# Kernel tuning notes

Hardware: AMD Instinct MI355X
Metric: run time of the kernel (lower is better)

The kernel has to match this reference:

```python
import jax, jax.numpy as jnp
import numpy as np
import math

B, S, E, HEAD = 4, 2048, 1024, 64  # num_heads=16 -> head_size = 1024//16


def setup_inputs() -> dict:
    key = jax.random.key(0)
    kx, kp, kq, kk, kv = jax.random.split(key, 5)
    std = math.sqrt(2.0 / (E + HEAD))
    return {
        "x": jax.random.normal(kx, (B, S, E), dtype=jnp.float32),
        "padding_mask": jax.random.randint(kp, (B, S), 0, 2, dtype=jnp.int32),
        "Wq": jax.random.normal(kq, (HEAD, E), dtype=jnp.float32) * std,
        "Wk": jax.random.normal(kk, (HEAD, E), dtype=jnp.float32) * std,
        "Wv": jax.random.normal(kv, (HEAD, E), dtype=jnp.float32) * std,
    }


def reference(x, padding_mask, Wq, Wk, Wv):
    # q,k,v: [B,S,head] via Linear (x @ W.T, no bias)
    q = jnp.einsum("bse,he->bsh", x, Wq)
    k = jnp.einsum("bse,he->bsh", x, Wk)
    v = jnp.einsum("bse,he->bsh", x, Wv)
    scores = jnp.einsum("bqh,bkh->bqk", q, k)  # [B,S,S]
    seq = x.shape[1]
    causal = jnp.tril(jnp.ones((seq, seq), dtype=jnp.float32))  # [S,S]
    mask = causal[None, :, :] * padding_mask.astype(jnp.float32)[:, None, :]  # [B,S,S]
    scores = jnp.where(mask == 0, jnp.float32(-1e9), scores)
    head_size = k.shape[-1]
    attn = jax.nn.softmax(scores / jnp.sqrt(jnp.float32(head_size)), axis=-1)
    return jnp.einsum("bqk,bkh->bqh", attn, v)
```

## Files before the change

kernel.cpp:

```cpp
#include <hip/hip_runtime.h>
#include <hip/hip_bf16.h>
#include <math.h>

#define B_ 4
#define S_ 2048
#define E_ 1024
#define H_ 64
#define NQT 32
#define SPLITS 8
#define TPS 4

typedef short bf16x8 __attribute__((ext_vector_type(8)));
typedef float f32x4 __attribute__((ext_vector_type(4)));
typedef unsigned short u16x8 __attribute__((ext_vector_type(8)));
typedef unsigned short u16x4 __attribute__((ext_vector_type(4)));

__device__ __forceinline__ unsigned short f2bf(float f){
    unsigned u = __builtin_bit_cast(unsigned, f);
    u += 0x7fffu + ((u >> 16) & 1u);
    return (unsigned short)(u >> 16);
}
__device__ __forceinline__ float bf2f(unsigned short h){
    return __builtin_bit_cast(float, ((unsigned)h) << 16);
}
#define MFMA16(a,b,c) __builtin_amdgcn_mfma_f32_16x16x32_bf16((a),(b),(c),0,0,0)

__device__ __forceinline__ void gload_lds16(const void* g, void* l){
    __builtin_amdgcn_global_load_lds((const __attribute__((address_space(1))) unsigned int*)g,
                                     (__attribute__((address_space(3))) unsigned int*)l, 16, 0, 0);
}

__global__ __launch_bounds__(256) void wprep_kernel(
    const float* __restrict__ Wq, const float* __restrict__ Wk,
    const float* __restrict__ Wv,
    unsigned short* __restrict__ WhiS, unsigned short* __restrict__ WloS)
{
    const int gid = blockIdx.x*256 + threadIdx.x;
    const int n = gid >> 7, g = gid & 127;
    const float* W = (n < 64)  ? (Wq + (size_t)n*E_)
                   : (n < 128) ? (Wk + (size_t)(n-64)*E_)
                               : (Wv + (size_t)(n-128)*E_);
    const int gs = (g & ~7) | ((g & 7) ^ (n & 7));
    const float* src = W + gs*8;
    float4 a = ((const float4*)src)[0];
    float4 b = ((const float4*)src)[1];
    float vv[8] = {a.x,a.y,a.z,a.w,b.x,b.y,b.z,b.w};
    u16x8 hv, lv;
    #pragma unroll
    for (int j=0;j<8;j++){ unsigned short h = f2bf(vv[j]); hv[j]=h; lv[j]=f2bf(vv[j]-bf2f(h)); }
    ((u16x8*)WhiS)[n*128 + g] = hv;
    ((u16x8*)WloS)[n*128 + g] = lv;
}

__global__ __launch_bounds__(256) void qkv_kernel(
    const float* __restrict__ x,
    const unsigned short* __restrict__ WhiS, const unsigned short* __restrict__ WloS,
    unsigned short* __restrict__ Qhi, unsigned short* __restrict__ Qlo,
    unsigned short* __restrict__ Khi, unsigned short* __restrict__ Klo,
    unsigned short* __restrict__ Vt)
{
    __shared__ unsigned short Ah[32*64], Al[32*64];
    __shared__ unsigned short Bh[192*64], Bl[192*64];
    const int m0 = blockIdx.x * 32;
    const int tid = threadIdx.x;
    const int lane = tid & 63, wv = tid >> 6, l15 = lane & 15, quad = lane >> 4;

    f32x4 acc[2][3];
    #pragma unroll
    for (int mt=0;mt<2;mt++)
    #pragma unroll
    for (int nt=0;nt<3;nt++) acc[mt][nt] = f32x4{0.f,0.f,0.f,0.f};

    const int arow = tid >> 3;
    const int ag   = tid & 7;
    unsigned short* tbuf = (wv < 2) ? Bh : Bl;
    const unsigned short* gsrc = (wv < 2) ? WhiS : WloS;
    const int rbase0 = (wv & 1) * 96;
    const int lrow = lane >> 3, lgrp = lane & 7;

    for (int k0 = 0; k0 < E_; k0 += 64) {
        const float* xs = x + (size_t)(m0 + arow)*E_ + k0 + ag*8;
        float4 xa = ((const float4*)xs)[0];
        float4 xb = ((const float4*)xs)[1];
        __syncthreads();
        #pragma unroll
        for (int i = 0; i < 12; i++) {
            const int rb = rbase0 + i*8;
            const unsigned short* gp = gsrc + (size_t)(rb + lrow)*E_ + k0 + lgrp*8;
            gload_lds16(gp, tbuf + rb*64);
        }
        {
            float vv[8] = {xa.x,xa.y,xa.z,xa.w,xb.x,xb.y,xb.z,xb.w};
            u16x8 hv, lv;
            #pragma unroll
            for (int j=0;j<8;j++){ unsigned short h = f2bf(vv[j]); hv[j]=h; lv[j]=f2bf(vv[j]-bf2f(h)); }
            const int idx = arow*8 + (ag ^ (arow & 7));
            ((u16x8*)Ah)[idx] = hv; ((u16x8*)Al)[idx] = lv;
        }
        __syncthreads();
        #pragma unroll
        for (int kk=0; kk<2; kk++){
            const int xr = (kk*4+quad) ^ (l15 & 7);
            bf16x8 ah[2], al[2];
            #pragma unroll
            for (int mt=0; mt<2; mt++){
                const int arw = mt*16 + l15;
                ah[mt] = ((const bf16x8*)Ah)[arw*8 + xr];
                al[mt] = ((const bf16x8*)Al)[arw*8 + xr];
            }
            #pragma unroll
            for (int nt=0; nt<3; nt++){
                const int brw = wv*48 + nt*16 + l15;
                bf16x8 bh = ((const bf16x8*)Bh)[brw*8 + xr];
                bf16x8 bl = ((const bf16x8*)Bl)[brw*8 + xr];
                #pragma unroll
                for (int mt=0; mt<2; mt++){
                    acc[mt][nt] = MFMA16(ah[mt], bh, acc[mt][nt]);
                    acc[mt][nt] = MFMA16(ah[mt], bl, acc[mt][nt]);
                    acc[mt][nt] = MFMA16(al[mt], bh, acc[mt][nt]);
                }
            }
        }
    }
    #pragma unroll
    for (int nt=0; nt<3; nt++){
        const int n = wv*48 + nt*16 + l15;
        const int comp = n >> 6, c = n & 63;
        if (comp < 2) {
            unsigned short* dh = (comp==0) ? Qhi : Khi;
            unsigned short* dl = (comp==0) ? Qlo : Klo;
            #pragma unroll
            for (int mt=0; mt<2; mt++)
            #pragma unroll
            for (int r=0; r<4; r++){
                const int row = m0 + mt*16 + quad*4 + r;
                float v = acc[mt][nt][r];
                unsigned short h = f2bf(v);
                dh[(size_t)row*H_ + c] = h;
                dl[(size_t)row*H_ + c] = f2bf(v - bf2f(h));
            }
        } else {
            #pragma unroll
            for (int mt=0; mt<2; mt++){
                const int m = m0 + mt*16 + quad*4;
                const int b = m >> 11, s0 = m & (S_-1);
                u16x4 pk;
                #pragma unroll
                for (int r=0;r<4;r++) pk[r] = f2bf(acc[mt][nt][r]);
                *(u16x4*)(Vt + (size_t)(b*H_ + c)*S_ + s0) = pk;
            }
        }
    }
}

__global__ __launch_bounds__(256) void meanv_kernel(const unsigned short* __restrict__ Vt,
                                                    float* __restrict__ meanV)
{
    int b = blockIdx.x >> 6, h = blockIdx.x & 63;
    const unsigned short* src = Vt + (size_t)b*H_*S_ + (size_t)h*S_;
    float sum = 0.f;
    for (int j = threadIdx.x; j < S_; j += 256) sum += bf2f(src[j]);
    #pragma unroll
    for (int m=32; m>=1; m>>=1) sum += __shfl_xor(sum, m);
    __shared__ float red[4];
    if ((threadIdx.x & 63) == 0) red[threadIdx.x >> 6] = sum;
    __syncthreads();
    if (threadIdx.x == 0) meanV[b*H_ + h] = (red[0]+red[1]+red[2]+red[3]) * (1.f/S_);
}

__global__ __launch_bounds__(256) void attn_kernel(
    const unsigned short* __restrict__ Qhi, const unsigned short* __restrict__ Qlo,
    const unsigned short* __restrict__ Khi, const unsigned short* __restrict__ Klo,
    const unsigned short* __restrict__ Vt, const int* __restrict__ pad,
    float* __restrict__ Opart, float* __restrict__ mpart, float* __restrict__ lpart)
{
    const int qt = blockIdx.x, b = blockIdx.y, sp = blockIdx.z;
    const int t0 = sp * TPS;
    if (t0 > qt) return;
    const int t1 = min(t0 + TPS, qt + 1);

    __shared__ unsigned short Ps[4][64*20];

    const int tid = threadIdx.x, lane = tid & 63, wv = tid >> 6, l15 = lane & 15, quad = lane >> 4;

    const size_t qrow = (size_t)(b*S_ + qt*64 + wv*16 + l15);
    bf16x8 aqh0 = *(const bf16x8*)(Qhi + qrow*H_ + quad*8);
    bf16x8 aqh1 = *(const bf16x8*)(Qhi + qrow*H_ + 32 + quad*8);
    bf16x8 aql0 = *(const bf16x8*)(Qlo + qrow*H_ + quad*8);
    bf16x8 aql1 = *(const bf16x8*)(Qlo + qrow*H_ + 32 + quad*8);

    const unsigned short* KhB = Khi + (size_t)(b*S_)*H_;
    const unsigned short* KlB = Klo + (size_t)(b*S_)*H_;
    const unsigned short* VB  = Vt  + (size_t)b*H_*S_;
    const int* padB = pad + b*S_;

    float m_i[4], l_i[4];
    f32x4 o[4];
    #pragma unroll
    for (int r=0;r<4;r++){ m_i[r] = -INFINITY; l_i[r] = 0.f; }
    #pragma unroll
    for (int i=0;i<4;i++) o[i] = f32x4{0.f,0.f,0.f,0.f};

    const int qg = qt*64 + wv*16 + quad*4;
    unsigned short* Pw = &Ps[wv][0];

    for (int t = t0; t < t1; ++t) {
        const int kb = t * 64;

        int pv[4];
        #pragma unroll
        for (int nt=0; nt<4; nt++) pv[nt] = padB[kb + nt*16 + l15];

        f32x4 s[4];
        #pragma unroll
        for (int nt=0; nt<4; nt++){
            const size_t krow = (size_t)(kb + nt*16 + l15)*H_;
            bf16x8 bh0 = *(const bf16x8*)(KhB + krow + quad*8);
            bf16x8 bh1 = *(const bf16x8*)(KhB + krow + 32 + quad*8);
            bf16x8 bl0 = *(const bf16x8*)(KlB + krow + quad*8);
            bf16x8 bl1 = *(const bf16x8*)(KlB + krow + 32 + quad*8);
            f32x4 z = f32x4{0.f,0.f,0.f,0.f};
            z = MFMA16(aqh0, bh0, z);
            z = MFMA16(aqh1, bh1, z);
            z = MFMA16(aqh0, bl0, z);
            z = MFMA16(aqh1, bl1, z);
            z = MFMA16(aql0, bh0, z);
            z = MFMA16(aql1, bh1, z);
            s[nt] = z;
        }
        float rmax[4] = {-INFINITY,-INFINITY,-INFINITY,-INFINITY};
        #pragma unroll
        for (int nt=0; nt<4; nt++){
            const int kg = kb + nt*16 + l15;
            #pragma unroll
            for (int r=0;r<4;r++){
                bool ok = (kg <= qg + r) && (pv[nt] != 0);
                float v = ok ? s[nt][r]*0.125f : -1.25e8f;
                s[nt][r] = v;
                rmax[r] = fmaxf(rmax[r], v);
            }
        }
        #pragma unroll
        for (int msk=1; msk<=8; msk<<=1){
            #pragma unroll
            for (int r=0;r<4;r++) rmax[r] = fmaxf(rmax[r], __shfl_xor(rmax[r], msk));
        }
        float alpha[4];
        #pragma unroll
        for (int r=0;r<4;r++){
            float mn = fmaxf(m_i[r], rmax[r]);
            alpha[r] = __expf(m_i[r] - mn);
            m_i[r] = mn;
        }
        float rsum[4] = {0.f,0.f,0.f,0.f};
        #pragma unroll
        for (int nt=0; nt<4; nt++)
        #pragma unroll
        for (int r=0;r<4;r++){
            float p = __expf(s[nt][r] - m_i[r]);
            s[nt][r] = p;
            rsum[r] += p;
        }
        #pragma unroll
        for (int msk=1; msk<=8; msk<<=1){
            #pragma unroll
            for (int r=0;r<4;r++) rsum[r] += __shfl_xor(rsum[r], msk);
        }
        #pragma unroll
        for (int r=0;r<4;r++) l_i[r] = l_i[r]*alpha[r] + rsum[r];
        #pragma unroll
        for (int hnt=0; hnt<4; hnt++)
        #pragma unroll
        for (int r=0;r<4;r++) o[hnt][r] *= alpha[r];

        #pragma unroll
        for (int nt=0; nt<4; nt++){
            const int key = nt*16 + l15;
            u16x4 pk;
            #pragma unroll
            for (int r=0;r<4;r++) pk[r] = f2bf(s[nt][r]);
            *(u16x4*)(Pw + key*20 + quad*4) = pk;
        }
        #pragma unroll
        for (int ks=0; ks<2; ks++){
            bf16x8 ap;
            #pragma unroll
            for (int j=0;j<8;j++) ap[j] = (short)Pw[(ks*32 + quad*8 + j)*20 + l15];
            #pragma unroll
            for (int hnt=0; hnt<4; hnt++){
                bf16x8 bv = *(const bf16x8*)(VB + (size_t)(hnt*16 + l15)*S_ + kb + ks*32 + quad*8);
                o[hnt] = MFMA16(ap, bv, o[hnt]);
            }
        }
    }
    const size_t rbase = ((size_t)((b*NQT + qt)*SPLITS + sp))*64 + wv*16 + quad*4;
    if (l15 == 0) {
        #pragma unroll
        for (int r=0;r<4;r++){ mpart[rbase + r] = m_i[r]; lpart[rbase + r] = l_i[r]; }
    }
    #pragma unroll
    for (int hnt=0; hnt<4; hnt++)
    #pragma unroll
    for (int r=0;r<4;r++)
        Opart[(rbase + r)*H_ + hnt*16 + l15] = o[hnt][r];
}

__global__ __launch_bounds__(256) void combine_kernel(
    const float* __restrict__ Opart, const float* __restrict__ mpart,
    const float* __restrict__ lpart, const float* __restrict__ meanV,
    float* __restrict__ out)
{
    const int idx = blockIdx.x*256 + threadIdx.x;
    const int h = idx & 63;
    const int q = (idx >> 6) & (S_-1);
    const int b = idx >> 17;
    const int qt = q >> 6, r = q & 63;
    const int ns = (qt >> 2) + 1;
    const size_t rb = ((size_t)(b*NQT + qt)*SPLITS)*64 + r;
    float M = -INFINITY;
    for (int s2=0; s2<ns; s2++) M = fmaxf(M, mpart[rb + (size_t)s2*64]);
    float res;
    if (M == -1.25e8f) {
        res = meanV[b*H_ + h];
    } else {
        float L = 0.f, acc = 0.f;
        for (int s2=0; s2<ns; s2++){
            float mi = mpart[rb + (size_t)s2*64];
            float wgt = __expf(mi - M);
            L += wgt * lpart[rb + (size_t)s2*64];
            acc += wgt * Opart[(rb + (size_t)s2*64)*H_ + h];
        }
        res = acc / L;
    }
    out[idx] = res;
}

extern "C" void kernel_launch(void* const* d_in, const int* in_sizes, int n_in,
                              void* d_out, int out_size, void* d_ws, size_t ws_size,
                              hipStream_t stream)
{
    (void)in_sizes; (void)n_in; (void)out_size; (void)ws_size;
    const float* x  = (const float*)d_in[0];
    const int* pad  = (const int*)d_in[1];
    const float* Wq = (const float*)d_in[2];
    const float* Wk = (const float*)d_in[3];
    const float* Wv = (const float*)d_in[4];
    float* out = (float*)d_out;
    char* ws = (char*)d_ws;
    const size_t MB = 1u << 20;
    unsigned short* Qhi = (unsigned short*)(ws + 0*MB);
    unsigned short* Qlo = (unsigned short*)(ws + 1*MB);
    unsigned short* Khi = (unsigned short*)(ws + 2*MB);
    unsigned short* Klo = (unsigned short*)(ws + 3*MB);
    unsigned short* Vt  = (unsigned short*)(ws + 4*MB);
    float* Opart = (float*)(ws + 5*MB);
    float* mpart = (float*)(ws + 21*MB);
    float* lpart = (float*)(ws + 21*MB + (1u<<18));
    float* meanV = (float*)(ws + 21*MB + 2*(1u<<18));
    unsigned short* WhiS = (unsigned short*)(ws + 22*MB);
    unsigned short* WloS = (unsigned short*)(ws + 22*MB + 512*1024);

    wprep_kernel<<<dim3(96), 256, 0, stream>>>(Wq, Wk, Wv, WhiS, WloS);
    qkv_kernel<<<dim3(256), 256, 0, stream>>>(x, WhiS, WloS, Qhi, Qlo, Khi, Klo, Vt);
    meanv_kernel<<<dim3(256), 256, 0, stream>>>(Vt, meanV);
    attn_kernel<<<dim3(NQT, B_, SPLITS), 256, 0, stream>>>(Qhi, Qlo, Khi, Klo, Vt, pad,
                                                           Opart, mpart, lpart);
    combine_kernel<<<dim3((B_*S_*H_)/256), 256, 0, stream>>>(Opart, mpart, lpart, meanV, out);
}
```

Baseline: 162.2 us.

## Double-buffer QKV and attention tiles in LDS, swizzle layouts, drop meanV kernel

The QKV projection now double-buffers its A and B tiles in LDS, so the loads for the next K-chunk overlap the MFMAs on the current one. The attention kernel stages the K hi/lo, V and padding tiles into LDS with per-wave roles, double-buffered, instead of reading fragments straight from global memory. Q, K and V are stored in XOR-swizzled layouts to cut LDS bank conflicts. The causal compare now runs only on the diagonal tile. The separate mean-V kernel is removed, and fully masked rows compute the V mean inline in the combine kernel, which is costly per thread but only for rare rows.

```diff
diff --git a/kernel.cpp b/kernel.cpp
--- a/kernel.cpp
+++ b/kernel.cpp
@@ -29,6 +29,7 @@
     __builtin_amdgcn_global_load_lds((const __attribute__((address_space(1))) unsigned int*)g,
                                      (__attribute__((address_space(3))) unsigned int*)l, 16, 0, 0);
 }
+
 
 __global__ __launch_bounds__(256) void wprep_kernel(
     const float* __restrict__ Wq, const float* __restrict__ Wk,
@@ -59,8 +60,8 @@
     unsigned short* __restrict__ Khi, unsigned short* __restrict__ Klo,
     unsigned short* __restrict__ Vt)
 {
-    __shared__ unsigned short Ah[32*64], Al[32*64];
-    __shared__ unsigned short Bh[192*64], Bl[192*64];
+    __shared__ unsigned short Ah[2][32*64], Al[2][32*64];
+    __shared__ unsigned short Bh[2][192*64], Bl[2][192*64];
     const int m0 = blockIdx.x * 32;
     const int tid = threadIdx.x;
     const int lane = tid & 63, wv = tid >> 6, l15 = lane & 15, quad = lane >> 4;
@@ -73,31 +74,39 @@
 
     const int arow = tid >> 3;
     const int ag   = tid & 7;
-    unsigned short* tbuf = (wv < 2) ? Bh : Bl;
     const unsigned short* gsrc = (wv < 2) ? WhiS : WloS;
     const int rbase0 = (wv & 1) * 96;
     const int lrow = lane >> 3, lgrp = lane & 7;
 
-    for (int k0 = 0; k0 < E_; k0 += 64) {
+    float4 xa, xb;
+    auto loadx = [&](int k0){
         const float* xs = x + (size_t)(m0 + arow)*E_ + k0 + ag*8;
-        float4 xa = ((const float4*)xs)[0];
-        float4 xb = ((const float4*)xs)[1];
-        __syncthreads();
+        xa = ((const float4*)xs)[0];
+        xb = ((const float4*)xs)[1];
+    };
+    auto stageB = [&](int buf, int k0){
+        unsigned short* tb = (wv < 2) ? &Bh[buf][0] : &Bl[buf][0];
         #pragma unroll
         for (int i = 0; i < 12; i++) {
             const int rb = rbase0 + i*8;
-            const unsigned short* gp = gsrc + (size_t)(rb + lrow)*E_ + k0 + lgrp*8;
-            gload_lds16(gp, tbuf + rb*64);
-        }
-        {
-            float vv[8] = {xa.x,xa.y,xa.z,xa.w,xb.x,xb.y,xb.z,xb.w};
-            u16x8 hv, lv;
-            #pragma unroll
-            for (int j=0;j<8;j++){ unsigned short h = f2bf(vv[j]); hv[j]=h; lv[j]=f2bf(vv[j]-bf2f(h)); }
-            const int idx = arow*8 + (ag ^ (arow & 7));
-            ((u16x8*)Ah)[idx] = hv; ((u16x8*)Al)[idx] = lv;
-        }
-        __syncthreads();
+            gload_lds16(gsrc + (size_t)(rb + lrow)*E_ + k0 + lgrp*8, tb + rb*64);
+        }
+    };
+    auto writeA = [&](int buf){
+        float vv[8] = {xa.x,xa.y,xa.z,xa.w,xb.x,xb.y,xb.z,xb.w};
+        u16x8 hv, lv;
+        #pragma unroll
+        for (int j=0;j<8;j++){ unsigned short h = f2bf(vv[j]); hv[j]=h; lv[j]=f2bf(vv[j]-bf2f(h)); }
+        const int idx = arow*8 + (ag ^ (arow & 7));
+        ((u16x8*)&Ah[buf][0])[idx] = hv; ((u16x8*)&Al[buf][0])[idx] = lv;
+    };
+
+    loadx(0); stageB(0, 0); writeA(0);
+    __syncthreads();
+
+    for (int k = 0; k < 16; k++) {
+        const int c = k & 1;
+        if (k < 15) { loadx((k+1)*64); stageB(c^1, (k+1)*64); }
         #pragma unroll
         for (int kk=0; kk<2; kk++){
             const int xr = (kk*4+quad) ^ (l15 & 7);
@@ -105,14 +114,14 @@
             #pragma unroll
             for (int mt=0; mt<2; mt++){
                 const int arw = mt*16 + l15;
-                ah[mt] = ((const bf16x8*)Ah)[arw*8 + xr];
-                al[mt] = ((const bf16x8*)Al)[arw*8 + xr];
+                ah[mt] = ((const bf16x8*)&Ah[c][0])[arw*8 + xr];
+                al[mt] = ((const bf16x8*)&Al[c][0])[arw*8 + xr];
             }
             #pragma unroll
             for (int nt=0; nt<3; nt++){
                 const int brw = wv*48 + nt*16 + l15;
-                bf16x8 bh = ((const bf16x8*)Bh)[brw*8 + xr];
-                bf16x8 bl = ((const bf16x8*)Bl)[brw*8 + xr];
+                bf16x8 bh = ((const bf16x8*)&Bh[c][0])[brw*8 + xr];
+                bf16x8 bl = ((const bf16x8*)&Bl[c][0])[brw*8 + xr];
                 #pragma unroll
                 for (int mt=0; mt<2; mt++){
                     acc[mt][nt] = MFMA16(ah[mt], bh, acc[mt][nt]);
@@ -121,11 +130,16 @@
                 }
             }
         }
+        if (k < 15) {
+            writeA(c^1);
+            __syncthreads();
+        }
     }
+
     #pragma unroll
     for (int nt=0; nt<3; nt++){
         const int n = wv*48 + nt*16 + l15;
-        const int comp = n >> 6, c = n & 63;
+        const int comp = n >> 6, cidx = n & 63;
         if (comp < 2) {
             unsigned short* dh = (comp==0) ? Qhi : Khi;
             unsigned short* dl = (comp==0) ? Qlo : Klo;
@@ -134,38 +148,26 @@
             #pragma unroll
             for (int r=0; r<4; r++){
                 const int row = m0 + mt*16 + quad*4 + r;
+                const int csw = (((cidx >> 3) ^ (row & 7)) << 3) | (cidx & 7);
                 float v = acc[mt][nt][r];
                 unsigned short h = f2bf(v);
-                dh[(size_t)row*H_ + c] = h;
-                dl[(size_t)row*H_ + c] = f2bf(v - bf2f(h));
+                dh[(size_t)row*H_ + csw] = h;
+                dl[(size_t)row*H_ + csw] = f2bf(v - bf2f(h));
             }
         } else {
             #pragma unroll
             for (int mt=0; mt<2; mt++){
                 const int m = m0 + mt*16 + quad*4;
                 const int b = m >> 11, s0 = m & (S_-1);
+                const int g = s0 >> 3;
+                const int pg = (g & ~7) | ((g ^ (cidx & 7)) & 7);
                 u16x4 pk;
                 #pragma unroll
                 for (int r=0;r<4;r++) pk[r] = f2bf(acc[mt][nt][r]);
-                *(u16x4*)(Vt + (size_t)(b*H_ + c)*S_ + s0) = pk;
+                *(u16x4*)(Vt + ((size_t)b*H_ + cidx)*S_ + pg*8 + (s0 & 7)) = pk;
             }
         }
     }
-}
-
-__global__ __launch_bounds__(256) void meanv_kernel(const unsigned short* __restrict__ Vt,
-                                                    float* __restrict__ meanV)
-{
-    int b = blockIdx.x >> 6, h = blockIdx.x & 63;
-    const unsigned short* src = Vt + (size_t)b*H_*S_ + (size_t)h*S_;
-    float sum = 0.f;
-    for (int j = threadIdx.x; j < S_; j += 256) sum += bf2f(src[j]);
-    #pragma unroll
-    for (int m=32; m>=1; m>>=1) sum += __shfl_xor(sum, m);
-    __shared__ float red[4];
-    if ((threadIdx.x & 63) == 0) red[threadIdx.x >> 6] = sum;
-    __syncthreads();
-    if (threadIdx.x == 0) meanV[b*H_ + h] = (red[0]+red[1]+red[2]+red[3]) * (1.f/S_);
 }
 
 __global__ __launch_bounds__(256) void attn_kernel(
@@ -179,15 +181,21 @@
     if (t0 > qt) return;
     const int t1 = min(t0 + TPS, qt + 1);
 
+    __shared__ unsigned short KtH[2][64*64], KtL[2][64*64], Vts[2][64*64];
     __shared__ unsigned short Ps[4][64*20];
+    __shared__ int pad_s[2][64];
 
     const int tid = threadIdx.x, lane = tid & 63, wv = tid >> 6, l15 = lane & 15, quad = lane >> 4;
+    const int role = wv;
 
     const size_t qrow = (size_t)(b*S_ + qt*64 + wv*16 + l15);
-    bf16x8 aqh0 = *(const bf16x8*)(Qhi + qrow*H_ + quad*8);
-    bf16x8 aqh1 = *(const bf16x8*)(Qhi + qrow*H_ + 32 + quad*8);
-    bf16x8 aql0 = *(const bf16x8*)(Qlo + qrow*H_ + quad*8);
-    bf16x8 aql1 = *(const bf16x8*)(Qlo + qrow*H_ + 32 + quad*8);
+    const int xk = l15 & 7;
+    const unsigned short* qbh = Qhi + qrow*H_;
+    const unsigned short* qbl = Qlo + qrow*H_;
+    bf16x8 aqh0 = *(const bf16x8*)(qbh + ((quad     ^ xk) << 3));
+    bf16x8 aqh1 = *(const bf16x8*)(qbh + (((4+quad) ^ xk) << 3));
+    bf16x8 aql0 = *(const bf16x8*)(qbl + ((quad     ^ xk) << 3));
+    bf16x8 aql1 = *(const bf16x8*)(qbl + (((4+quad) ^ xk) << 3));
 
     const unsigned short* KhB = Khi + (size_t)(b*S_)*H_;
     const unsigned short* KlB = Klo + (size_t)(b*S_)*H_;
@@ -204,21 +212,50 @@
     const int qg = qt*64 + wv*16 + quad*4;
     unsigned short* Pw = &Ps[wv][0];
 
+    auto stage = [&](int buf, int t){
+        const int kb = t * 64;
+        if (role == 0){
+            const unsigned short* g = KhB + (size_t)kb*H_;
+            unsigned short* l = &KtH[buf][0];
+            #pragma unroll
+            for (int j=0;j<8;j++) gload_lds16(g + j*512 + lane*8, l + j*512);
+        } else if (role == 1){
+            const unsigned short* g = KlB + (size_t)kb*H_;
+            unsigned short* l = &KtL[buf][0];
+            #pragma unroll
+            for (int j=0;j<8;j++) gload_lds16(g + j*512 + lane*8, l + j*512);
+        } else if (role == 2){
+            unsigned short* l = &Vts[buf][0];
+            const unsigned short* g = VB + (size_t)(lane>>3)*S_ + kb + (lane&7)*8;
+            #pragma unroll
+            for (int j=0;j<8;j++) gload_lds16(g + (size_t)j*8*S_, l + j*512);
+        } else {
+            pad_s[buf][lane] = padB[kb + lane];
+        }
+    };
+
+    stage(0, t0);
+    __syncthreads();
+
     for (int t = t0; t < t1; ++t) {
+        const int c = (t - t0) & 1;
         const int kb = t * 64;
+        if (t + 1 < t1) stage(c^1, t+1);
 
         int pv[4];
         #pragma unroll
-        for (int nt=0; nt<4; nt++) pv[nt] = padB[kb + nt*16 + l15];
-
+        for (int nt=0; nt<4; nt++) pv[nt] = pad_s[c][nt*16 + l15];
+
+        const bf16x8* KH = (const bf16x8*)&KtH[c][0];
+        const bf16x8* KL = (const bf16x8*)&KtL[c][0];
         f32x4 s[4];
         #pragma unroll
         for (int nt=0; nt<4; nt++){
-            const size_t krow = (size_t)(kb + nt*16 + l15)*H_;
-            bf16x8 bh0 = *(const bf16x8*)(KhB + krow + quad*8);
-            bf16x8 bh1 = *(const bf16x8*)(KhB + krow + 32 + quad*8);
-            bf16x8 bl0 = *(const bf16x8*)(KlB + krow + quad*8);
-            bf16x8 bl1 = *(const bf16x8*)(KlB + krow + 32 + quad*8);
+            const int krw = nt*16 + l15;
+            bf16x8 bh0 = KH[krw*8 + ((quad)   ^ xk)];
+            bf16x8 bh1 = KH[krw*8 + ((4+quad) ^ xk)];
+            bf16x8 bl0 = KL[krw*8 + ((quad)   ^ xk)];
+            bf16x8 bl1 = KL[krw*8 + ((4+quad) ^ xk)];
             f32x4 z = f32x4{0.f,0.f,0.f,0.f};
             z = MFMA16(aqh0, bh0, z);
             z = MFMA16(aqh1, bh1, z);
@@ -229,15 +266,28 @@
             s[nt] = z;
         }
         float rmax[4] = {-INFINITY,-INFINITY,-INFINITY,-INFINITY};
-        #pragma unroll
-        for (int nt=0; nt<4; nt++){
-            const int kg = kb + nt*16 + l15;
-            #pragma unroll
-            for (int r=0;r<4;r++){
-                bool ok = (kg <= qg + r) && (pv[nt] != 0);
-                float v = ok ? s[nt][r]*0.125f : -1.25e8f;
-                s[nt][r] = v;
-                rmax[r] = fmaxf(rmax[r], v);
+        if (t == qt) {
+            #pragma unroll
+            for (int nt=0; nt<4; nt++){
+                const int kg = kb + nt*16 + l15;
+                #pragma unroll
+                for (int r=0;r<4;r++){
+                    bool ok = (kg <= qg + r) && (pv[nt] != 0);
+                    float v = ok ? s[nt][r]*0.125f : -1.25e8f;
+                    s[nt][r] = v;
+                    rmax[r] = fmaxf(rmax[r], v);
+                }
+            }
+        } else {
+            #pragma unroll
+            for (int nt=0; nt<4; nt++){
+                const bool ok = (pv[nt] != 0);
+                #pragma unroll
+                for (int r=0;r<4;r++){
+                    float v = ok ? s[nt][r]*0.125f : -1.25e8f;
+                    s[nt][r] = v;
+                    rmax[r] = fmaxf(rmax[r], v);
+                }
             }
         }
         #pragma unroll
@@ -281,6 +331,7 @@
             for (int r=0;r<4;r++) pk[r] = f2bf(s[nt][r]);
             *(u16x4*)(Pw + key*20 + quad*4) = pk;
         }
+        const bf16x8* VS = (const bf16x8*)&Vts[c][0];
         #pragma unroll
         for (int ks=0; ks<2; ks++){
             bf16x8 ap;
@@ -288,10 +339,12 @@
             for (int j=0;j<8;j++) ap[j] = (short)Pw[(ks*32 + quad*8 + j)*20 + l15];
             #pragma unroll
             for (int hnt=0; hnt<4; hnt++){
-                bf16x8 bv = *(const bf16x8*)(VB + (size_t)(hnt*16 + l15)*S_ + kb + ks*32 + quad*8);
+                bf16x8 bv = VS[(hnt*16+l15)*8 + ((ks*4+quad) ^ xk)];
                 o[hnt] = MFMA16(ap, bv, o[hnt]);
             }
         }
+
+        if (t + 1 < t1) __syncthreads();
     }
     const size_t rbase = ((size_t)((b*NQT + qt)*SPLITS + sp))*64 + wv*16 + quad*4;
     if (l15 == 0) {
@@ -307,7 +360,7 @@
 
 __global__ __launch_bounds__(256) void combine_kernel(
     const float* __restrict__ Opart, const float* __restrict__ mpart,
-    const float* __restrict__ lpart, const float* __restrict__ meanV,
+    const float* __restrict__ lpart, const unsigned short* __restrict__ Vt,
     float* __restrict__ out)
 {
     const int idx = blockIdx.x*256 + threadIdx.x;
@@ -321,7 +374,15 @@
     for (int s2=0; s2<ns; s2++) M = fmaxf(M, mpart[rb + (size_t)s2*64]);
     float res;
     if (M == -1.25e8f) {
-        res = meanV[b*H_ + h];
+        const unsigned short* src = Vt + ((size_t)b*H_ + h)*S_;
+        float sum = 0.f;
+        #pragma unroll 4
+        for (int j=0;j<256;j++){
+            u16x8 d = ((const u16x8*)src)[j];
+            #pragma unroll
+            for (int e=0;e<8;e++) sum += bf2f((unsigned short)d[e]);
+        }
+        res = sum * (1.f/(float)S_);
     } else {
         float L = 0.f, acc = 0.f;
         for (int s2=0; s2<ns; s2++){
@@ -356,14 +417,12 @@
     float* Opart = (float*)(ws + 5*MB);
     float* mpart = (float*)(ws + 21*MB);
     float* lpart = (float*)(ws + 21*MB + (1u<<18));
-    float* meanV = (float*)(ws + 21*MB + 2*(1u<<18));
     unsigned short* WhiS = (unsigned short*)(ws + 22*MB);
     unsigned short* WloS = (unsigned short*)(ws + 22*MB + 512*1024);
 
     wprep_kernel<<<dim3(96), 256, 0, stream>>>(Wq, Wk, Wv, WhiS, WloS);
     qkv_kernel<<<dim3(256), 256, 0, stream>>>(x, WhiS, WloS, Qhi, Qlo, Khi, Klo, Vt);
-    meanv_kernel<<<dim3(256), 256, 0, stream>>>(Vt, meanV);
     attn_kernel<<<dim3(NQT, B_, SPLITS), 256, 0, stream>>>(Qhi, Qlo, Khi, Klo, Vt, pad,
                                                            Opart, mpart, lpart);
-    combine_kernel<<<dim3((B_*S_*H_)/256), 256, 0, stream>>>(Opart, mpart, lpart, meanV, out);
-}
+    combine_kernel<<<dim3((B_*S_*H_)/256), 256, 0, stream>>>(Opart, mpart, lpart, Vt, out);
+}
```

After: 147.7 us. -8.9%, faster.
